# Kernel tuning notes

Hardware: AMD Instinct MI355X
Metric: run time of the kernel (lower is better)

Reference implementation:

```python
import jax, jax.numpy as jnp
from jax import lax
import numpy as np

B, T, N, F_IN, H, E, K = 8, 32, 500, 64, 128, 8000, 3
LN_EPS = 1e-5


def setup_inputs() -> dict:
    key = jax.random.key(0)
    ks = jax.random.split(key, 10)
    x = jax.random.normal(ks[0], (B, T, N, F_IN), dtype=jnp.float32)
    edge_index = jax.random.randint(ks[1], (2, E), 0, N, dtype=jnp.int64)
    edge_weight = jax.random.uniform(ks[2], (E,), dtype=jnp.float32)
    # GCNConv: linear (in->out) + bias
    W_gcn = jax.random.normal(ks[3], (F_IN, H), dtype=jnp.float32) / np.sqrt(F_IN)
    b_gcn = jnp.zeros((H,), dtype=jnp.float32)
    # Conv1d(H, H, K): weight (O, I, K)
    W_temp = jax.random.normal(ks[4], (H, H, K), dtype=jnp.float32) / np.sqrt(H * K)
    b_temp = jnp.zeros((H,), dtype=jnp.float32)
    # LayerNorm(H)
    ln_w = jnp.ones((H,), dtype=jnp.float32)
    ln_b = jnp.zeros((H,), dtype=jnp.float32)
    # residual Linear (in->out)
    W_res = jax.random.normal(ks[5], (F_IN, H), dtype=jnp.float32) / np.sqrt(F_IN)
    b_res = jnp.zeros((H,), dtype=jnp.float32)
    return {"x": x, "edge_index": edge_index, "edge_weight": edge_weight,
            "W_gcn": W_gcn, "b_gcn": b_gcn, "W_temp": W_temp, "b_temp": b_temp,
            "ln_w": ln_w, "ln_b": ln_b, "W_res": W_res, "b_res": b_res}


def reference(x, edge_index, edge_weight, W_gcn, b_gcn, W_temp, b_temp, ln_w, ln_b, W_res, b_res):
    Bv, Tv, Nv, Fv = x.shape
    Hv = W_gcn.shape[1]
    res = x @ W_res + b_res  # (B,T,N,H)

    # ---- spatial GCNConv on B*T replicated graphs (vectorized, no index offsetting) ----
    xf = x.reshape(Bv * Tv, Nv, Fv) @ W_gcn  # (BT,N,H)
    src, dst = edge_index[0], edge_index[1]
    loops = jnp.arange(Nv, dtype=edge_index.dtype)
    src2 = jnp.concatenate([src, loops])
    dst2 = jnp.concatenate([dst, loops])
    ew2 = jnp.concatenate([edge_weight, jnp.ones((Nv,), dtype=edge_weight.dtype)])
    deg = jax.ops.segment_sum(ew2, dst2, num_segments=Nv)
    dinv = jnp.where(deg > 0, deg ** -0.5, 0.0)
    norm = dinv[src2] * ew2 * dinv[dst2]  # (E+N,)
    msgs = xf[:, src2, :] * norm[None, :, None]  # (BT, E+N, H)
    agg = jax.vmap(lambda m: jax.ops.segment_sum(m, dst2, num_segments=Nv))(msgs)
    h = jax.nn.gelu(agg + b_gcn, approximate=False)  # (BT,N,H)

    # ---- temporal Conv1d over T ----
    h = h.reshape(Bv, Tv, Nv, Hv).transpose(0, 2, 3, 1).reshape(Bv * Nv, Hv, Tv)
    pad = K // 2
    h = lax.conv_general_dilated(h, W_temp, window_strides=(1,), padding=[(pad, pad)],
                                 dimension_numbers=("NCH", "OIH", "NCH"))
    h = jax.nn.gelu(h + b_temp[None, :, None], approximate=False)
    h = h.reshape(Bv, Nv, Hv, Tv).transpose(0, 3, 1, 2)  # (B,T,N,H)

    # ---- fused residual + LayerNorm over last dim ----
    y = h + res
    mu = jnp.mean(y, axis=-1, keepdims=True)
    var = jnp.mean((y - mu) ** 2, axis=-1, keepdims=True)
    return (y - mu) * lax.rsqrt(var + LN_EPS) * ln_w + ln_b
```

## Files before the change

### kernel.cpp

```cpp
#include <hip/hip_runtime.h>
#include <hip/hip_bf16.h>
#include <math.h>

#define Bv 8
#define Tv 32
#define Nv 500
#define NP 512
#define Fin 64
#define Hv 128
#define Ev 8000
#define Kv 3
#define BT (Bv*Tv)
#define ROWS (BT*Nv)
#define NCOL (BT*Fin)
#define TP (Tv+2)
#define KK (Kv*Hv)
#define LDSROW 144

typedef __attribute__((ext_vector_type(8))) short s8v;
typedef __attribute__((ext_vector_type(4))) float f4v;

__device__ __forceinline__ float gelu_exact(float v){
    float t  = v*0.70710678118654752440f;
    float ax = fabsf(t);
    float k  = __builtin_amdgcn_rcpf(fmaf(0.3275911f, ax, 1.0f));
    float p  = k*fmaf(k, fmaf(k, fmaf(k, fmaf(k, 1.061405429f, -1.453152027f),
                                      1.421413741f), -0.284496736f), 0.254829592f);
    float e  = __expf(-ax*ax);
    float er = fmaf(-p, e, 1.0f);
    er = copysignf(er, t);
    return 0.5f*v*(1.0f + er);
}
__device__ __forceinline__ short f2bs(float f){
    union { __hip_bfloat16 h; short s; } u;
    u.h = __float2bfloat16(f);
    return u.s;
}

__global__ __launch_bounds__(256) void k_t(const float* __restrict__ x,
        short* __restrict__ XT, float* __restrict__ Af32,
        const float* __restrict__ W, const float* __restrict__ Wg,
        const float* __restrict__ Wr,
        short* __restrict__ W2, short* __restrict__ Wgt, short* __restrict__ Wrt,
        const int* __restrict__ ei, const float* __restrict__ ew,
        float* __restrict__ dinv){
    int bid = blockIdx.x;
    int tid = threadIdx.x;
    if (bid < 2048){
        __shared__ short t[64][72];
        int bt = bid >> 3;
        int n0 = (bid & 7) * 64;
        int r   = tid >> 2;
        int c16 = (tid & 3) * 16;
        int n = n0 + r;
        short sv[16];
        if (n < Nv){
            const float4* src = (const float4*)(x + ((size_t)bt*Nv + n)*64 + c16);
            #pragma unroll
            for (int j = 0; j < 4; ++j){
                float4 v = src[j];
                sv[j*4+0]=f2bs(v.x); sv[j*4+1]=f2bs(v.y);
                sv[j*4+2]=f2bs(v.z); sv[j*4+3]=f2bs(v.w);
            }
        } else {
            #pragma unroll
            for (int j = 0; j < 16; ++j) sv[j] = 0;
        }
        #pragma unroll
        for (int j = 0; j < 16; ++j) t[r][c16+j] = sv[j];
        __syncthreads();
        int cc  = tid >> 2;
        int nn0 = (tid & 3) * 16;
        short ov[16];
        #pragma unroll
        for (int j = 0; j < 16; ++j) ov[j] = t[nn0+j][cc];
        short* dst = XT + (size_t)(bt*64 + cc)*NP + n0 + nn0;
        *(s8v*)dst       = *(s8v*)&ov[0];
        *(s8v*)(dst + 8) = *(s8v*)&ov[8];
    } else if (bid == 2048){
        __shared__ float sdeg[Nv];
        for (int i = tid; i < Nv; i += 256) sdeg[i] = 1.0f;
        __syncthreads();
        for (int e = tid; e < Ev; e += 256)
            atomicAdd(&sdeg[ei[Ev + e]], ew[e]);
        __syncthreads();
        for (int i = tid; i < Nv; i += 256){
            float d = sdeg[i];
            dinv[i] = (d > 0.f) ? rsqrtf(d) : 0.f;
        }
    } else if (bid <= 2304){
        int i = (bid-2049)*256 + tid;
        ((float4*)Af32)[i] = make_float4(0.f,0.f,0.f,0.f);
    } else {
        int idx = (bid-2305)*256 + tid;
        if (idx < Hv*Hv*Kv){
            int o = idx/(Hv*Kv);
            int rem = idx - o*(Hv*Kv);
            int i = rem/Kv, k = rem - i*Kv;
            W2[o*KK + k*Hv + i] = f2bs(W[idx]);
        } else if (idx < Hv*Hv*Kv + Hv*64){
            int j = idx - Hv*Hv*Kv;
            int o = j >> 6, k = j & 63;
            Wgt[j] = f2bs(Wg[k*Hv + o]);
        } else if (idx < Hv*Hv*Kv + 2*Hv*64){
            int j = idx - Hv*Hv*Kv - Hv*64;
            int o = j >> 6, k = j & 63;
            Wrt[j] = f2bs(Wr[k*Hv + o]);
        }
    }
}

__global__ __launch_bounds__(1024) void k_scat(const int* __restrict__ ei,
        const float* __restrict__ ew, const float* __restrict__ dinv,
        float* __restrict__ Af32){
    int e = blockIdx.x*1024 + threadIdx.x;
    if (e < Ev){
        int s = ei[e], d = ei[Ev + e];
        atomicAdd(&Af32[(size_t)d*NP + s], dinv[s]*ew[e]*dinv[d]);
    }
    if (blockIdx.x == 0 && threadIdx.x < Nv){
        float dv = dinv[threadIdx.x];
        atomicAdd(&Af32[(size_t)threadIdx.x*NP + threadIdx.x], dv*dv);
    }
}

__global__ __launch_bounds__(1024) void k_cvt(const float* __restrict__ Af32,
        short* __restrict__ Ab){
    int i = blockIdx.x*1024 + threadIdx.x;
    float4 v = ((const float4*)Af32)[i];
    short4 s;
    s.x = f2bs(v.x); s.y = f2bs(v.y); s.z = f2bs(v.z); s.w = f2bs(v.w);
    ((short4*)Ab)[i] = s;
}

__global__ __launch_bounds__(256) void k_gemm(const short* __restrict__ Ab,
        const short* __restrict__ XT, short* __restrict__ AGG2){
    int tid  = threadIdx.x;
    int w    = tid >> 6;
    int lane = tid & 63;
    int quad = lane >> 4;
    int laneo = lane & 15;
    int bid = blockIdx.x;
    int jt = bid & 127, it = bid >> 7;
    int i0 = it*128;
    int j0 = jt*128 + w*32;

    f4v acc[8][2];
    #pragma unroll
    for (int m = 0; m < 8; ++m){
        acc[m][0] = (f4v){0.f,0.f,0.f,0.f};
        acc[m][1] = (f4v){0.f,0.f,0.f,0.f};
    }
    #pragma unroll 2
    for (int ks = 0; ks < 16; ++ks){
        int k0 = ks*32 + quad*8;
        s8v bfr[2];
        #pragma unroll
        for (int nt = 0; nt < 2; ++nt)
            bfr[nt] = *(const s8v*)(XT + (size_t)(j0 + nt*16 + laneo)*NP + k0);
        #pragma unroll
        for (int m = 0; m < 8; ++m){
            s8v afr = *(const s8v*)(Ab + (size_t)(i0 + m*16 + laneo)*NP + k0);
            acc[m][0] = __builtin_amdgcn_mfma_f32_16x16x32_bf16(afr, bfr[0], acc[m][0], 0,0,0);
            acc[m][1] = __builtin_amdgcn_mfma_f32_16x16x32_bf16(afr, bfr[1], acc[m][1], 0,0,0);
        }
    }
    #pragma unroll
    for (int m = 0; m < 8; ++m){
        #pragma unroll
        for (int r = 0; r < 4; ++r){
            int row = i0 + m*16 + quad*4 + r;
            if (row < Nv){
                #pragma unroll
                for (int nt = 0; nt < 2; ++nt)
                    AGG2[(size_t)row*NCOL + j0 + nt*16 + laneo] = f2bs(acc[m][nt][r]);
            }
        }
    }
}

__global__ __launch_bounds__(256, 2) void k_mega(
        const short* __restrict__ AGG2, const float* __restrict__ x,
        const short* __restrict__ W2, const short* __restrict__ Wgt,
        const short* __restrict__ Wrt,
        const float* __restrict__ bg, const float* __restrict__ btm,
        const float* __restrict__ br, const float* __restrict__ lw,
        const float* __restrict__ lb, float* __restrict__ out){
    __shared__ short hs[4*TP*LDSROW];
    __shared__ float red[Tv][4][2];
    int tid  = threadIdx.x;
    int w    = tid >> 6;
    int lane = tid & 63;
    int quad = lane >> 4;
    int laneo = lane & 15;
    int bid = blockIdx.x;
    int b  = bid / 125;
    int n0 = (bid - b*125) * 4;
    int o_base = w*32;

    float bgv[2], bbv[2], brv[2], lwv[2], lbv[2];
    #pragma unroll
    for (int nt = 0; nt < 2; ++nt){
        int o = o_base + nt*16 + laneo;
        bgv[nt] = bg[o]; bbv[nt] = btm[o]; brv[nt] = br[o];
        lwv[nt] = lw[o]; lbv[nt] = lb[o];
    }

    s8v bwg[2][2];
    #pragma unroll
    for (int nt = 0; nt < 2; ++nt){
        const short* wp = Wgt + (o_base + nt*16 + laneo)*64 + quad*8;
        bwg[nt][0] = *(const s8v*)wp;
        bwg[nt][1] = *(const s8v*)(wp + 32);
    }

    if (tid < 128){
        int node = tid >> 5, rem = tid & 31;
        int tp = (rem >> 4)*(TP-1), c8 = rem & 15;
        s8v z = {0,0,0,0,0,0,0,0};
        *(s8v*)&hs[node*(TP*LDSROW) + tp*LDSROW + c8*8] = z;
    }

    for (int g = 0; g < 4; ++g){
        int n = n0 + g;
        const short* ap = AGG2 + ((size_t)n*BT + b*Tv)*64;
        #pragma unroll
        for (int m = 0; m < 2; ++m){
            const short* arp = ap + (m*16 + laneo)*64 + quad*8;
            s8v a0 = *(const s8v*)arp;
            s8v a1 = *(const s8v*)(arp + 32);
            f4v h0 = {0.f,0.f,0.f,0.f}, h1 = {0.f,0.f,0.f,0.f};
            h0 = __builtin_amdgcn_mfma_f32_16x16x32_bf16(a0, bwg[0][0], h0, 0,0,0);
            h0 = __builtin_amdgcn_mfma_f32_16x16x32_bf16(a1, bwg[0][1], h0, 0,0,0);
            h1 = __builtin_amdgcn_mfma_f32_16x16x32_bf16(a0, bwg[1][0], h1, 0,0,0);
            h1 = __builtin_amdgcn_mfma_f32_16x16x32_bf16(a1, bwg[1][1], h1, 0,0,0);
            #pragma unroll
            for (int r = 0; r < 4; ++r){
                int tp = m*16 + quad*4 + r + 1;
                short* hrow = &hs[g*(TP*LDSROW) + tp*LDSROW];
                hrow[o_base + laneo]      = f2bs(gelu_exact(h0[r] + bgv[0]));
                hrow[o_base + 16 + laneo] = f2bs(gelu_exact(h1[r] + bgv[1]));
            }
        }
    }

    s8v breg[2][12], bwr[2][2];
    #pragma unroll
    for (int nt = 0; nt < 2; ++nt){
        int o = o_base + nt*16 + laneo;
        const short* wp = W2 + o*KK + quad*8;
        #pragma unroll
        for (int s = 0; s < 12; ++s)
            breg[nt][s] = *(const s8v*)(wp + s*32);
        const short* wr = Wrt + o*64 + quad*8;
        bwr[nt][0] = *(const s8v*)wr;
        bwr[nt][1] = *(const s8v*)(wr + 32);
    }
    __syncthreads();

    for (int g = 0; g < 4; ++g){
        int n = n0 + g;
        f4v acc[2][2];
        #pragma unroll
        for (int m = 0; m < 2; ++m)
            #pragma unroll
            for (int nt = 0; nt < 2; ++nt)
                acc[m][nt] = (f4v){0.f,0.f,0.f,0.f};
        #pragma unroll
        for (int m = 0; m < 2; ++m){
            #pragma unroll
            for (int s = 0; s < 12; ++s){
                int k  = s >> 2;
                int i0 = (s & 3) * 32;
                int tp = m*16 + laneo + k;
                s8v a = *(const s8v*)&hs[g*(TP*LDSROW) + tp*LDSROW + i0 + quad*8];
                acc[m][0] = __builtin_amdgcn_mfma_f32_16x16x32_bf16(a, breg[0][s], acc[m][0], 0,0,0);
                acc[m][1] = __builtin_amdgcn_mfma_f32_16x16x32_bf16(a, breg[1][s], acc[m][1], 0,0,0);
            }
        }
        f4v racc[2][2];
        #pragma unroll
        for (int m = 0; m < 2; ++m)
            #pragma unroll
            for (int nt = 0; nt < 2; ++nt)
                racc[m][nt] = (f4v){0.f,0.f,0.f,0.f};
        #pragma unroll
        for (int m = 0; m < 2; ++m){
            const float* xr = x + (((size_t)(b*Tv + m*16 + laneo))*Nv + n)*64 + quad*8;
            float4 f0 = *(const float4*)xr;
            float4 f1 = *(const float4*)(xr + 4);
            float4 f2 = *(const float4*)(xr + 32);
            float4 f3 = *(const float4*)(xr + 36);
            s8v a0, a1;
            a0[0]=f2bs(f0.x); a0[1]=f2bs(f0.y); a0[2]=f2bs(f0.z); a0[3]=f2bs(f0.w);
            a0[4]=f2bs(f1.x); a0[5]=f2bs(f1.y); a0[6]=f2bs(f1.z); a0[7]=f2bs(f1.w);
            a1[0]=f2bs(f2.x); a1[1]=f2bs(f2.y); a1[2]=f2bs(f2.z); a1[3]=f2bs(f2.w);
            a1[4]=f2bs(f3.x); a1[5]=f2bs(f3.y); a1[6]=f2bs(f3.z); a1[7]=f2bs(f3.w);
            racc[m][0] = __builtin_amdgcn_mfma_f32_16x16x32_bf16(a0, bwr[0][0], racc[m][0], 0,0,0);
            racc[m][0] = __builtin_amdgcn_mfma_f32_16x16x32_bf16(a1, bwr[0][1], racc[m][0], 0,0,0);
            racc[m][1] = __builtin_amdgcn_mfma_f32_16x16x32_bf16(a0, bwr[1][0], racc[m][1], 0,0,0);
            racc[m][1] = __builtin_amdgcn_mfma_f32_16x16x32_bf16(a1, bwr[1][1], racc[m][1], 0,0,0);
        }
        size_t obase = ((size_t)b*Tv*Nv + n)*Hv;
        float yv[2][2][4];
        float srow[2][4], ssrow[2][4];
        #pragma unroll
        for (int m = 0; m < 2; ++m)
            #pragma unroll
            for (int r = 0; r < 4; ++r){ srow[m][r] = 0.f; ssrow[m][r] = 0.f; }
        #pragma unroll
        for (int m = 0; m < 2; ++m){
            #pragma unroll
            for (int nt = 0; nt < 2; ++nt){
                #pragma unroll
                for (int r = 0; r < 4; ++r){
                    float gv = gelu_exact(acc[m][nt][r] + bbv[nt]);
                    float y = gv + racc[m][nt][r] + brv[nt];
                    yv[m][nt][r] = y;
                    srow[m][r] += y; ssrow[m][r] += y*y;
                }
            }
        }
        #pragma unroll
        for (int m = 0; m < 2; ++m)
            #pragma unroll
            for (int r = 0; r < 4; ++r){
                #pragma unroll
                for (int msk = 8; msk >= 1; msk >>= 1){
                    srow[m][r]  += __shfl_xor(srow[m][r],  msk, 64);
                    ssrow[m][r] += __shfl_xor(ssrow[m][r], msk, 64);
                }
            }
        if (laneo == 0){
            #pragma unroll
            for (int m = 0; m < 2; ++m)
                #pragma unroll
                for (int r = 0; r < 4; ++r){
                    int t = m*16 + quad*4 + r;
                    red[t][w][0] = srow[m][r];
                    red[t][w][1] = ssrow[m][r];
                }
        }
        __syncthreads();
        #pragma unroll
        for (int m = 0; m < 2; ++m){
            #pragma unroll
            for (int r = 0; r < 4; ++r){
                int t = m*16 + quad*4 + r;
                float s  = red[t][0][0] + red[t][1][0] + red[t][2][0] + red[t][3][0];
                float ss = red[t][0][1] + red[t][1][1] + red[t][2][1] + red[t][3][1];
                float mu = s * (1.f/128.f);
                float var = fmaxf(ss * (1.f/128.f) - mu*mu, 0.f);
                float rstd = rsqrtf(var + 1e-5f);
                #pragma unroll
                for (int nt = 0; nt < 2; ++nt){
                    int o = o_base + nt*16 + laneo;
                    out[obase + (size_t)t*Nv*Hv + o] =
                        (yv[m][nt][r] - mu)*rstd*lwv[nt] + lbv[nt];
                }
            }
        }
        __syncthreads();
    }
}

extern "C" void kernel_launch(void* const* d_in, const int* in_sizes, int n_in,
                              void* d_out, int out_size, void* d_ws, size_t ws_size,
                              hipStream_t stream){
    const float* x   = (const float*)d_in[0];
    const int*   ei  = (const int*)d_in[1];
    const float* ew  = (const float*)d_in[2];
    const float* Wg  = (const float*)d_in[3];
    const float* bg  = (const float*)d_in[4];
    const float* Wtm = (const float*)d_in[5];
    const float* btm = (const float*)d_in[6];
    const float* lw  = (const float*)d_in[7];
    const float* lb  = (const float*)d_in[8];
    const float* Wr  = (const float*)d_in[9];
    const float* br  = (const float*)d_in[10];
    float* out = (float*)d_out;

    char* ws = (char*)d_ws;
    float* dinv = (float*)(ws + 0);
    float* Af32 = (float*)(ws + 4096);
    short* Ab   = (short*)(ws + 1052672);
    short* W2   = (short*)(ws + 1576960);
    short* Wgt  = (short*)(ws + 1675264);
    short* Wrt  = (short*)(ws + 1691648);
    short* XT   = (short*)(ws + 1708032);
    short* AGG2 = (short*)(ws + 18485248);

    k_t   <<<2561, 256, 0, stream>>>(x, XT, Af32, Wtm, Wg, Wr,
                                     W2, Wgt, Wrt, ei, ew, dinv);
    k_scat<<<8, 1024, 0, stream>>>(ei, ew, dinv, Af32);
    k_cvt <<<64, 1024, 0, stream>>>(Af32, Ab);
    k_gemm<<<512, 256, 0, stream>>>(Ab, XT, AGG2);
    k_mega<<<(Bv*Nv)/4, 256, 0, stream>>>(AGG2, x, W2, Wgt, Wrt,
                                          bg, btm, br, lw, lb, out);
}
```

Measured before the change: 220.9 us.

## Fuse adjacency build into prep kernel and feed residual from bf16 node-major copy

Replaces the separate scatter and convert kernels with per-block row construction of the normalized adjacency in shared memory: each of 32 blocks recomputes the degrees and builds 16 rows directly in bf16, which removes two launches and the fp32 staging buffer. The prep kernel also writes a node-major bf16 copy of x, so the mega kernel reads contiguous bf16 residual operands instead of strided fp32 loads with conversion. The mega kernel's occupancy hint is raised from 2 to 3 blocks per CU. The cost is redundant degree computation and edge scans in every adjacency block, about 16 MB of extra bf16 writes, and possible register pressure from the tighter launch bound.

```diff
diff --git a/kernel.cpp b/kernel.cpp
--- a/kernel.cpp
+++ b/kernel.cpp
@@ -11,7 +11,6 @@
 #define Ev 8000
 #define Kv 3
 #define BT (Bv*Tv)
-#define ROWS (BT*Nv)
 #define NCOL (BT*Fin)
 #define TP (Tv+2)
 #define KK (Kv*Hv)
@@ -37,13 +36,12 @@
     return u.s;
 }
 
-__global__ __launch_bounds__(256) void k_t(const float* __restrict__ x,
-        short* __restrict__ XT, float* __restrict__ Af32,
+__global__ __launch_bounds__(256) void k_prep(const float* __restrict__ x,
+        short* __restrict__ XT, short* __restrict__ X2b, short* __restrict__ Ab,
         const float* __restrict__ W, const float* __restrict__ Wg,
         const float* __restrict__ Wr,
         short* __restrict__ W2, short* __restrict__ Wgt, short* __restrict__ Wrt,
-        const int* __restrict__ ei, const float* __restrict__ ew,
-        float* __restrict__ dinv){
+        const int* __restrict__ ei, const float* __restrict__ ew){
     int bid = blockIdx.x;
     int tid = threadIdx.x;
     if (bid < 2048){
@@ -62,6 +60,9 @@
                 sv[j*4+0]=f2bs(v.x); sv[j*4+1]=f2bs(v.y);
                 sv[j*4+2]=f2bs(v.z); sv[j*4+3]=f2bs(v.w);
             }
+            short* xb = X2b + (size_t)n*NCOL + bt*64 + c16;
+            *(s8v*)xb       = *(s8v*)&sv[0];
+            *(s8v*)(xb + 8) = *(s8v*)&sv[8];
         } else {
             #pragma unroll
             for (int j = 0; j < 16; ++j) sv[j] = 0;
@@ -77,22 +78,47 @@
         short* dst = XT + (size_t)(bt*64 + cc)*NP + n0 + nn0;
         *(s8v*)dst       = *(s8v*)&ov[0];
         *(s8v*)(dst + 8) = *(s8v*)&ov[8];
-    } else if (bid == 2048){
-        __shared__ float sdeg[Nv];
-        for (int i = tid; i < Nv; i += 256) sdeg[i] = 1.0f;
+    } else if (bid < 2080){
+        __shared__ float deg[Nv];
+        __shared__ float rowbuf[16*NP];
+        int r0 = (bid - 2048)*16;
+        for (int i = tid; i < Nv; i += 256) deg[i] = 1.0f;
+        for (int i = tid; i < 16*NP; i += 256) rowbuf[i] = 0.f;
         __syncthreads();
         for (int e = tid; e < Ev; e += 256)
-            atomicAdd(&sdeg[ei[Ev + e]], ew[e]);
+            atomicAdd(&deg[ei[Ev + e]], ew[e]);
         __syncthreads();
         for (int i = tid; i < Nv; i += 256){
-            float d = sdeg[i];
-            dinv[i] = (d > 0.f) ? rsqrtf(d) : 0.f;
-        }
-    } else if (bid <= 2304){
-        int i = (bid-2049)*256 + tid;
-        ((float4*)Af32)[i] = make_float4(0.f,0.f,0.f,0.f);
+            float d = deg[i];
+            deg[i] = (d > 0.f) ? rsqrtf(d) : 0.f;
+        }
+        __syncthreads();
+        for (int e = tid; e < Ev; e += 256){
+            int d = ei[Ev + e];
+            unsigned g = (unsigned)(d - r0);
+            if (g < 16u){
+                int s = ei[e];
+                atomicAdd(&rowbuf[g*NP + s], deg[s]*ew[e]*deg[d]);
+            }
+        }
+        __syncthreads();
+        if (tid < 16){
+            int row = r0 + tid;
+            if (row < Nv){
+                float dv = deg[row];
+                rowbuf[tid*NP + row] += dv*dv;
+            }
+        }
+        __syncthreads();
+        for (int i = tid; i < 16*NP/8; i += 256){
+            const float* rp = &rowbuf[i*8];
+            s8v o;
+            #pragma unroll
+            for (int j = 0; j < 8; ++j) o[j] = f2bs(rp[j]);
+            *(s8v*)(Ab + (size_t)r0*NP + i*8) = o;
+        }
     } else {
-        int idx = (bid-2305)*256 + tid;
+        int idx = (bid - 2080)*256 + tid;
         if (idx < Hv*Hv*Kv){
             int o = idx/(Hv*Kv);
             int rem = idx - o*(Hv*Kv);
@@ -110,29 +136,6 @@
     }
 }
 
-__global__ __launch_bounds__(1024) void k_scat(const int* __restrict__ ei,
-        const float* __restrict__ ew, const float* __restrict__ dinv,
-        float* __restrict__ Af32){
-    int e = blockIdx.x*1024 + threadIdx.x;
-    if (e < Ev){
-        int s = ei[e], d = ei[Ev + e];
-        atomicAdd(&Af32[(size_t)d*NP + s], dinv[s]*ew[e]*dinv[d]);
-    }
-    if (blockIdx.x == 0 && threadIdx.x < Nv){
-        float dv = dinv[threadIdx.x];
-        atomicAdd(&Af32[(size_t)threadIdx.x*NP + threadIdx.x], dv*dv);
-    }
-}
-
-__global__ __launch_bounds__(1024) void k_cvt(const float* __restrict__ Af32,
-        short* __restrict__ Ab){
-    int i = blockIdx.x*1024 + threadIdx.x;
-    float4 v = ((const float4*)Af32)[i];
-    short4 s;
-    s.x = f2bs(v.x); s.y = f2bs(v.y); s.z = f2bs(v.z); s.w = f2bs(v.w);
-    ((short4*)Ab)[i] = s;
-}
-
 __global__ __launch_bounds__(256) void k_gemm(const short* __restrict__ Ab,
         const short* __restrict__ XT, short* __restrict__ AGG2){
     int tid  = threadIdx.x;
@@ -179,8 +182,8 @@
     }
 }
 
-__global__ __launch_bounds__(256, 2) void k_mega(
-        const short* __restrict__ AGG2, const float* __restrict__ x,
+__global__ __launch_bounds__(256, 3) void k_mega(
+        const short* __restrict__ AGG2, const short* __restrict__ X2b,
         const short* __restrict__ W2, const short* __restrict__ Wgt,
         const short* __restrict__ Wrt,
         const float* __restrict__ bg, const float* __restrict__ btm,
@@ -284,18 +287,12 @@
             #pragma unroll
             for (int nt = 0; nt < 2; ++nt)
                 racc[m][nt] = (f4v){0.f,0.f,0.f,0.f};
-        #pragma unroll
-        for (int m = 0; m < 2; ++m){
-            const float* xr = x + (((size_t)(b*Tv + m*16 + laneo))*Nv + n)*64 + quad*8;
-            float4 f0 = *(const float4*)xr;
-            float4 f1 = *(const float4*)(xr + 4);
-            float4 f2 = *(const float4*)(xr + 32);
-            float4 f3 = *(const float4*)(xr + 36);
-            s8v a0, a1;
-            a0[0]=f2bs(f0.x); a0[1]=f2bs(f0.y); a0[2]=f2bs(f0.z); a0[3]=f2bs(f0.w);
-            a0[4]=f2bs(f1.x); a0[5]=f2bs(f1.y); a0[6]=f2bs(f1.z); a0[7]=f2bs(f1.w);
-            a1[0]=f2bs(f2.x); a1[1]=f2bs(f2.y); a1[2]=f2bs(f2.z); a1[3]=f2bs(f2.w);
-            a1[4]=f2bs(f3.x); a1[5]=f2bs(f3.y); a1[6]=f2bs(f3.z); a1[7]=f2bs(f3.w);
+        const short* xp = X2b + ((size_t)n*BT + b*Tv)*64;
+        #pragma unroll
+        for (int m = 0; m < 2; ++m){
+            const short* xrp = xp + (m*16 + laneo)*64 + quad*8;
+            s8v a0 = *(const s8v*)xrp;
+            s8v a1 = *(const s8v*)(xrp + 32);
             racc[m][0] = __builtin_amdgcn_mfma_f32_16x16x32_bf16(a0, bwr[0][0], racc[m][0], 0,0,0);
             racc[m][0] = __builtin_amdgcn_mfma_f32_16x16x32_bf16(a1, bwr[0][1], racc[m][0], 0,0,0);
             racc[m][1] = __builtin_amdgcn_mfma_f32_16x16x32_bf16(a0, bwr[1][0], racc[m][1], 0,0,0);
@@ -381,20 +378,17 @@
     float* out = (float*)d_out;
 
     char* ws = (char*)d_ws;
-    float* dinv = (float*)(ws + 0);
-    float* Af32 = (float*)(ws + 4096);
-    short* Ab   = (short*)(ws + 1052672);
-    short* W2   = (short*)(ws + 1576960);
-    short* Wgt  = (short*)(ws + 1675264);
-    short* Wrt  = (short*)(ws + 1691648);
-    short* XT   = (short*)(ws + 1708032);
-    short* AGG2 = (short*)(ws + 18485248);
-
-    k_t   <<<2561, 256, 0, stream>>>(x, XT, Af32, Wtm, Wg, Wr,
-                                     W2, Wgt, Wrt, ei, ew, dinv);
-    k_scat<<<8, 1024, 0, stream>>>(ei, ew, dinv, Af32);
-    k_cvt <<<64, 1024, 0, stream>>>(Af32, Ab);
+    short* Ab   = (short*)(ws + 0);
+    short* W2   = (short*)(ws + 524288);
+    short* Wgt  = (short*)(ws + 622592);
+    short* Wrt  = (short*)(ws + 638976);
+    short* X2b  = (short*)(ws + 655360);
+    short* XT   = (short*)(ws + 17039360);
+    short* AGG2 = (short*)(ws + 33816576);
+
+    k_prep<<<2336, 256, 0, stream>>>(x, XT, X2b, Ab, Wtm, Wg, Wr,
+                                     W2, Wgt, Wrt, ei, ew);
     k_gemm<<<512, 256, 0, stream>>>(Ab, XT, AGG2);
-    k_mega<<<(Bv*Nv)/4, 256, 0, stream>>>(AGG2, x, W2, Wgt, Wrt,
+    k_mega<<<(Bv*Nv)/4, 256, 0, stream>>>(AGG2, X2b, W2, Wgt, Wrt,
                                           bg, btm, br, lw, lb, out);
 }
```

Result: slower. 258.1 us (+16.8%).
